# Kernel tuning notes

Measured on AMD Instinct MI355X. Metric: run time of the kernel, lower is better.

The kernel has to match this reference:

```python
import jax, jax.numpy as jnp
import numpy as np

B, S, C = 8, 4096, 256
K = 8192  # num_embeddings


def setup_inputs() -> dict:
    key = jax.random.key(0)
    k1, k2 = jax.random.split(key)
    inputs = jax.random.normal(k1, (B, S, C), dtype=jnp.float32)
    # torch init: uniform_(-1/K, 1/K)
    weight = jax.random.uniform(k2, (K, C), dtype=jnp.float32, minval=-1.0 / K, maxval=1.0 / K)
    return {"inputs": inputs, "weight": weight}


def reference(inputs, weight):
    b, s, c = inputs.shape
    flat = inputs.reshape(b * s, c)                       # (N, C)
    distances = (
        jnp.sum(flat * flat, axis=1, keepdims=True)
        + jnp.sum(weight * weight, axis=1)
        - 2.0 * jnp.matmul(flat, weight.T)
    )
    encoding_indices = jnp.argmin(distances, axis=1)      # (N,)
    quantized = weight[encoding_indices].reshape(b, s, c)  # gather == one-hot matmul
    encoding_indices = encoding_indices.reshape(b, s)
    # straight-through estimator
    quantized = inputs + jax.lax.stop_gradient(quantized - inputs)
    return quantized, encoding_indices
```

## Files before the change

kernel.cpp:

```cpp
#include <hip/hip_runtime.h>
#include <hip/hip_fp16.h>

#define N_ROWS 32768
#define KCODES 8192
#define CDIM   256
#define NSUB   (KCODES / 16)
#define MARGIN_DOT 2.2e-4f
#define CAP_ROW 15
#define CAP_BIN 1024

typedef __attribute__((ext_vector_type(8))) short bf16x8;
typedef __attribute__((ext_vector_type(4))) float f32x4;

#define GLOAD_LDS16(g, l)                                                              \
    __builtin_amdgcn_global_load_lds((const __attribute__((address_space(1))) void*)(g), \
                                     (__attribute__((address_space(3))) void*)(l), 16, 0, 0)

__device__ __forceinline__ ushort f2bf_rne(float f) {
    unsigned u = __float_as_uint(f);
    u += 0x7fffu + ((u >> 16) & 1u);
    return (ushort)(u >> 16);
}

__global__ void prep_kernel(const float* __restrict__ x, const float* __restrict__ wgt,
                            ushort* __restrict__ xb, ushort* __restrict__ wb,
                            float* __restrict__ t1, float* __restrict__ e2,
                            unsigned long long* __restrict__ bestG) {
    const int gtid = blockIdx.x * blockDim.x + threadIdx.x;
    if (gtid < N_ROWS) bestG[gtid] = ~0ull;

    int wave = gtid >> 6;
    int lane = threadIdx.x & 63;
    const float* src; ushort* bdst; float* sqdst; int row;
    if (wave < N_ROWS) { src = x; bdst = xb; sqdst = t1; row = wave; }
    else               { src = wgt; bdst = wb; sqdst = e2; row = wave - N_ROWS; }
    float4 v = *((const float4*)src + (size_t)row * (CDIM / 4) + lane);
    ushort4 o;
    o.x = f2bf_rne(v.x); o.y = f2bf_rne(v.y); o.z = f2bf_rne(v.z); o.w = f2bf_rne(v.w);
    *((ushort4*)bdst + (size_t)row * (CDIM / 4) + lane) = o;
    float s = v.x * v.x + v.y * v.y + v.z * v.z + v.w * v.w;
    for (int off = 32; off; off >>= 1) s += __shfl_down(s, off, 64);
    if (lane == 0) sqdst[row] = s;
}

__launch_bounds__(512, 3)
__global__ void vq_mfma_kernel(const ushort* __restrict__ xb, const ushort* __restrict__ wb,
                               __half* __restrict__ minT) {
    __shared__ ushort xs[2][256 * 32];
    __shared__ ushort ws_l[2][128 * 32];
    ushort (*mbT)[264] = (ushort (*)[264])&xs[0][0];

    const int t = threadIdx.x;
    const int w = t >> 6, lane = t & 63;
    const int ln15 = lane & 15, quad = lane >> 4;
    const int rt = blockIdx.x >> 6;
    const int ct = blockIdx.x & 63;
    const int rbase = (w >> 1) * 64;
    const int cbase = (w & 1) * 64;

    const int srow16 = lane >> 2;
    const int schunk = (lane & 3) ^ ((lane >> 3) & 3);
    const ushort* xsrc = xb + (size_t)(rt * 256 + w * 32 + srow16) * CDIM + schunk * 8;
    const ushort* wsrc = wb + (size_t)(ct * 128 + w * 16 + srow16) * CDIM + schunk * 8;

    f32x4 acc[4][4];
#pragma unroll
    for (int ni = 0; ni < 4; ++ni)
#pragma unroll
        for (int mi = 0; mi < 4; ++mi)
#pragma unroll
            for (int r = 0; r < 4; ++r) acc[ni][mi][r] = 0.f;

#pragma unroll
    for (int j = 0; j < 2; ++j)
        GLOAD_LDS16(xsrc + (size_t)j * 16 * CDIM, &xs[0][(w * 32 + j * 16) * 32]);
    GLOAD_LDS16(wsrc, &ws_l[0][(w * 16) * 32]);
    __syncthreads();

#pragma unroll
    for (int cc = 0; cc < 8; ++cc) {
        const int cur = cc & 1;
        if (cc < 7) {
#pragma unroll
            for (int j = 0; j < 2; ++j)
                GLOAD_LDS16(xsrc + (size_t)j * 16 * CDIM + (cc + 1) * 32,
                            &xs[cur ^ 1][(w * 32 + j * 16) * 32]);
            GLOAD_LDS16(wsrc + (cc + 1) * 32, &ws_l[cur ^ 1][(w * 16) * 32]);
        }
        const int swz = (quad ^ ((ln15 >> 1) & 3)) * 8;
        bf16x8 a[4], b[4];
#pragma unroll
        for (int ni = 0; ni < 4; ++ni)
            a[ni] = *(const bf16x8*)&ws_l[cur][(cbase + ni * 16 + ln15) * 32 + swz];
#pragma unroll
        for (int mi = 0; mi < 4; ++mi)
            b[mi] = *(const bf16x8*)&xs[cur][(rbase + mi * 16 + ln15) * 32 + swz];
#pragma unroll
        for (int ni = 0; ni < 4; ++ni)
#pragma unroll
            for (int mi = 0; mi < 4; ++mi)
                acc[ni][mi] = __builtin_amdgcn_mfma_f32_16x16x32_bf16(a[ni], b[mi], acc[ni][mi], 0, 0, 0);
        __syncthreads();
    }

#pragma unroll
    for (int mi = 0; mi < 4; ++mi) {
        float mxn[4];
#pragma unroll
        for (int ni = 0; ni < 4; ++ni) {
            f32x4 v = acc[ni][mi];
            float mx = fmaxf(fmaxf(v[0], v[1]), fmaxf(v[2], v[3]));
            mx = fmaxf(mx, __shfl_xor(mx, 16, 64));
            mx = fmaxf(mx, __shfl_xor(mx, 32, 64));
            mxn[ni] = mx;
        }
        float sel = quad == 0 ? mxn[0] : quad == 1 ? mxn[1] : quad == 2 ? mxn[2] : mxn[3];
        uint pk = __builtin_bit_cast(uint, __builtin_amdgcn_cvt_pkrtz(sel, sel));
        mbT[(cbase >> 4) + quad][rbase + mi * 16 + ln15] = (ushort)(pk & 0xffffu);
    }
    __syncthreads();
    if (t < 256) {
        union { ushort s[8]; uint4 u; } r;
#pragma unroll
        for (int s = 0; s < 8; ++s) r.s[s] = mbT[s][t];
        *(uint4*)(minT + ((size_t)(rt * 64 + ct) * 256 + t) * 8) = r.u;
    }
}

__launch_bounds__(256, 8)
__global__ void vq_scan_kernel(const __half* __restrict__ minT, uint* __restrict__ rowcand) {
    __shared__ ushort sm[64][136];
    __shared__ ushort cand[16][16];
    const int t = threadIdx.x, w = t >> 6, lane = t & 63;
    const int row0 = blockIdx.x * 16;

    {
        const int ct = t >> 2, c4 = t & 3;
        const uint4* src = (const uint4*)(minT +
            ((((size_t)(row0 >> 8) * 64 + ct) * 256 + (row0 & 255) + c4 * 4) * 8));
#pragma unroll
        for (int i = 0; i < 4; ++i)
            *(uint4*)&sm[ct][(c4 * 4 + i) * 8] = src[i];
    }
    __syncthreads();

    for (int i = 0; i < 4; ++i) {
        const int rr = w * 4 + i;
        union { uint4 u; __half2 h2[4]; } raw;
        raw.u = *(const uint4*)&sm[lane][rr * 8];
        float m[8];
#pragma unroll
        for (int q = 0; q < 4; ++q) {
            float2 f = __half22float2(raw.h2[q]);
            m[2 * q] = f.x;
            m[2 * q + 1] = f.y;
        }
        float lmax = m[0];
#pragma unroll
        for (int q = 1; q < 8; ++q) lmax = fmaxf(lmax, m[q]);
#pragma unroll
        for (int off = 1; off < 64; off <<= 1) lmax = fmaxf(lmax, __shfl_xor(lmax, off, 64));
        const float thresh = lmax - MARGIN_DOT;

        int base = 0;
#pragma unroll
        for (int s = 0; s < 8; ++s) {
            bool c = (m[s] >= thresh);
            unsigned long long mask = __ballot(c);
            if (c) {
                int pos = base + (int)__popcll(mask & ((1ull << lane) - 1ull));
                if (pos < CAP_ROW) cand[rr][1 + pos] = (ushort)(lane * 8 + s);
            }
            base += (int)__popcll(mask);
        }
        if (lane == 0) cand[rr][0] = (base <= CAP_ROW) ? (ushort)base : (ushort)0xffff;
    }
    __syncthreads();
    if (t < 128)
        rowcand[(size_t)(row0 + (t >> 3)) * 8 + (t & 7)] = ((const uint*)cand)[t];
}

__launch_bounds__(512, 4)
__global__ void vq_subproc_kernel(const float* __restrict__ x, const float* __restrict__ wgt,
                                  const float* __restrict__ t1, const float* __restrict__ e2,
                                  const uint* __restrict__ rowcand,
                                  unsigned long long* __restrict__ bestG) {
    __shared__ float wsub[16][260];
    __shared__ float xbuf[32][264];
    __shared__ int list[CAP_BIN];
    __shared__ int nlist;

    const int t = threadIdx.x;
    const int g = t >> 4, gl = t & 15;
    const int st = blockIdx.x;

    if (t == 0) nlist = 0;
#pragma unroll
    for (int j = 0; j < 2; ++j) {
        const int idx = t + 512 * j;
        *(float4*)&wsub[idx >> 6][(idx & 63) * 4] =
            ((const float4*)(wgt + (size_t)(st * 16 + (idx >> 6)) * CDIM))[idx & 63];
    }
    const float e2v = e2[st * 16 + gl];
    __syncthreads();

    for (int it = 0; it < 64; ++it) {
        const int r = t + 512 * it;
        union { struct { uint4 a, b; } qq; ushort h[16]; } rc;
        rc.qq.a = ((const uint4*)rowcand)[(size_t)r * 2];
        rc.qq.b = ((const uint4*)rowcand)[(size_t)r * 2 + 1];
        const uint cnt = rc.h[0];
        bool match = (cnt == 0xffffu);
        const int n = cnt < (uint)CAP_ROW ? (int)cnt : CAP_ROW;
#pragma unroll
        for (int j = 0; j < CAP_ROW; ++j)
            match |= (j < n) && (rc.h[1 + j] == (ushort)st);
        if (match) {
            const int pos = atomicAdd(&nlist, 1);
            if (pos < CAP_BIN) {
                list[pos] = r;
            } else {
                const float* xp = x + (size_t)r * CDIM;
                const float t1r = t1[r];
                unsigned long long bk = ~0ull;
                for (int kk = 0; kk < 16; ++kk) {
                    float acc = 0.f;
                    for (int c = 0; c < CDIM; ++c) acc = fmaf(xp[c], wsub[kk][c], acc);
                    float d = (t1r + e2[st * 16 + kk]) - 2.0f * acc;
                    unsigned long long key =
                        ((unsigned long long)__float_as_uint(d) << 32) | (uint)(st * 16 + kk);
                    bk = key < bk ? key : bk;
                }
                atomicMin(&bestG[r], bk);
            }
        }
    }
    __syncthreads();

    const int cnt = nlist < CAP_BIN ? nlist : CAP_BIN;
    for (int base = 0; base < cnt; base += 32) {
        const int e = base + g;
        const bool valid = e < cnt;
        int row = 0;
        if (valid) {
            row = list[e];
            const float4* xs = (const float4*)(x + (size_t)row * CDIM);
#pragma unroll
            for (int j = 0; j < 4; ++j)
                *(float4*)&xbuf[g][(gl + 16 * j) * 4] = xs[gl + 16 * j];
        }
        unsigned long long key = ~0ull;
        if (valid) {
            float acc = 0.f;
#pragma unroll
            for (int c4 = 0; c4 < 64; ++c4) {
                const float4 wv = *(const float4*)&wsub[gl][c4 * 4];
                const float4 xv = *(const float4*)&xbuf[g][c4 * 4];
                acc = fmaf(xv.x, wv.x, acc);
                acc = fmaf(xv.y, wv.y, acc);
                acc = fmaf(xv.z, wv.z, acc);
                acc = fmaf(xv.w, wv.w, acc);
            }
            const int k = st * 16 + gl;
            float d = (t1[row] + e2v) - 2.0f * acc;
            key = ((unsigned long long)__float_as_uint(d) << 32) | (uint)k;
        }
#pragma unroll
        for (int off = 1; off < 16; off <<= 1) {
            unsigned long long ok = __shfl_xor(key, off, 64);
            key = ok < key ? ok : key;
        }
        if (gl == 0 && valid) atomicMin(&bestG[row], key);
    }
}

__launch_bounds__(256, 8)
__global__ void vq_gather_kernel(const float* __restrict__ wgt,
                                 const unsigned long long* __restrict__ bestG,
                                 float* __restrict__ out_q, float* __restrict__ out_i) {
    const int t = threadIdx.x;
    const int g = t >> 4, gl = t & 15;
    const int row = blockIdx.x * 16 + g;
    const int bk = (int)(uint)(bestG[row] & 0xffffffffu);
    if (gl == 0) out_i[row] = (float)bk;
    const float4* src = (const float4*)(wgt + (size_t)bk * CDIM);
    float4* dst = (float4*)(out_q + (size_t)row * CDIM);
#pragma unroll
    for (int j = 0; j < 4; ++j) dst[gl + 16 * j] = src[gl + 16 * j];
}

extern "C" void kernel_launch(void* const* d_in, const int* in_sizes, int n_in,
                              void* d_out, int out_size, void* d_ws, size_t ws_size,
                              hipStream_t stream) {
    const float* x = (const float*)d_in[0];
    const float* wgt = (const float*)d_in[1];

    float* out_q = (float*)d_out;
    float* out_i = out_q + (size_t)N_ROWS * CDIM;

    char* p = (char*)d_ws;
    float* e2 = (float*)p;                     p += (size_t)KCODES * 4;
    float* t1 = (float*)p;                     p += (size_t)N_ROWS * 4;
    __half* minT = (__half*)p;                 p += (size_t)N_ROWS * NSUB * 2;
    ushort* xb = (ushort*)p;                   p += (size_t)N_ROWS * CDIM * 2;
    ushort* wb = (ushort*)p;                   p += (size_t)KCODES * CDIM * 2;
    unsigned long long* bestG = (unsigned long long*)p; p += (size_t)N_ROWS * 8;
    uint* rowcand = (uint*)p;                  p += (size_t)N_ROWS * 32;

    prep_kernel<<<(N_ROWS + KCODES) / 4, 256, 0, stream>>>(x, wgt, xb, wb, t1, e2, bestG);
    vq_mfma_kernel<<<(N_ROWS / 256) * (KCODES / 128), 512, 0, stream>>>(xb, wb, minT);
    vq_scan_kernel<<<N_ROWS / 16, 256, 0, stream>>>(minT, rowcand);
    vq_subproc_kernel<<<NSUB, 512, 0, stream>>>(x, wgt, t1, e2, rowcand, bestG);
    vq_gather_kernel<<<N_ROWS / 16, 256, 0, stream>>>(wgt, bestG, out_q, out_i);
}
```

Measured before the change: 347.1 us.

## Replace per-row candidate lists with row thresholds and split subproc over rows

The scan kernel now only computes a per-row threshold (row max minus margin) instead of building capped candidate lists. The subproc kernel reads the minT sub-block maxima and the threshold directly to decide whether a row belongs to its 16-code subtile. Its grid is split four ways over rows to raise parallelism. This removes the candidate-list writes and the 15-way compare loop per row, and removes the per-row cap that forced overflow rows into every subtile. In exchange, each subproc block does strided 16-byte reads from minT and an extra threshold load per row.

```diff
diff --git a/kernel.cpp b/kernel.cpp
--- a/kernel.cpp
+++ b/kernel.cpp
@@ -6,8 +6,8 @@
 #define CDIM   256
 #define NSUB   (KCODES / 16)
 #define MARGIN_DOT 2.2e-4f
-#define CAP_ROW 15
 #define CAP_BIN 1024
+#define SPLIT  4
 
 typedef __attribute__((ext_vector_type(8))) short bf16x8;
 typedef __attribute__((ext_vector_type(4))) float f32x4;
@@ -128,9 +128,8 @@
 }
 
 __launch_bounds__(256, 8)
-__global__ void vq_scan_kernel(const __half* __restrict__ minT, uint* __restrict__ rowcand) {
+__global__ void vq_rowmax_kernel(const __half* __restrict__ minT, float* __restrict__ thresh) {
     __shared__ ushort sm[64][136];
-    __shared__ ushort cand[16][16];
     const int t = threadIdx.x, w = t >> 6, lane = t & 63;
     const int row0 = blockIdx.x * 16;
 
@@ -160,30 +159,15 @@
         for (int q = 1; q < 8; ++q) lmax = fmaxf(lmax, m[q]);
 #pragma unroll
         for (int off = 1; off < 64; off <<= 1) lmax = fmaxf(lmax, __shfl_xor(lmax, off, 64));
-        const float thresh = lmax - MARGIN_DOT;
-
-        int base = 0;
-#pragma unroll
-        for (int s = 0; s < 8; ++s) {
-            bool c = (m[s] >= thresh);
-            unsigned long long mask = __ballot(c);
-            if (c) {
-                int pos = base + (int)__popcll(mask & ((1ull << lane) - 1ull));
-                if (pos < CAP_ROW) cand[rr][1 + pos] = (ushort)(lane * 8 + s);
-            }
-            base += (int)__popcll(mask);
-        }
-        if (lane == 0) cand[rr][0] = (base <= CAP_ROW) ? (ushort)base : (ushort)0xffff;
-    }
-    __syncthreads();
-    if (t < 128)
-        rowcand[(size_t)(row0 + (t >> 3)) * 8 + (t & 7)] = ((const uint*)cand)[t];
+        if (lane == 0) thresh[row0 + rr] = lmax - MARGIN_DOT;
+    }
 }
 
 __launch_bounds__(512, 4)
 __global__ void vq_subproc_kernel(const float* __restrict__ x, const float* __restrict__ wgt,
                                   const float* __restrict__ t1, const float* __restrict__ e2,
-                                  const uint* __restrict__ rowcand,
+                                  const __half* __restrict__ minT,
+                                  const float* __restrict__ thresh,
                                   unsigned long long* __restrict__ bestG) {
     __shared__ float wsub[16][260];
     __shared__ float xbuf[32][264];
@@ -192,7 +176,9 @@
 
     const int t = threadIdx.x;
     const int g = t >> 4, gl = t & 15;
-    const int st = blockIdx.x;
+    const int st = blockIdx.x >> 2;
+    const int sp = blockIdx.x & (SPLIT - 1);
+    const int ct = st >> 3, sub = st & 7;
 
     if (t == 0) nlist = 0;
 #pragma unroll
@@ -204,18 +190,15 @@
     const float e2v = e2[st * 16 + gl];
     __syncthreads();
 
-    for (int it = 0; it < 64; ++it) {
-        const int r = t + 512 * it;
-        union { struct { uint4 a, b; } qq; ushort h[16]; } rc;
-        rc.qq.a = ((const uint4*)rowcand)[(size_t)r * 2];
-        rc.qq.b = ((const uint4*)rowcand)[(size_t)r * 2 + 1];
-        const uint cnt = rc.h[0];
-        bool match = (cnt == 0xffffu);
-        const int n = cnt < (uint)CAP_ROW ? (int)cnt : CAP_ROW;
-#pragma unroll
-        for (int j = 0; j < CAP_ROW; ++j)
-            match |= (j < n) && (rc.h[1 + j] == (ushort)st);
-        if (match) {
+    for (int it = 0; it < 16; ++it) {
+        const int r = sp * (N_ROWS / SPLIT) + t + 512 * it;
+        const uint4 mg = *(const uint4*)(minT +
+            ((((size_t)(r >> 8) * 64 + ct) * 256 + (r & 255)) * 8));
+        const uint word = (sub >> 1) == 0 ? mg.x : (sub >> 1) == 1 ? mg.y
+                        : (sub >> 1) == 2 ? mg.z : mg.w;
+        const ushort hbits = (sub & 1) ? (ushort)(word >> 16) : (ushort)(word & 0xffffu);
+        const float ms = __half2float(__builtin_bit_cast(__half, hbits));
+        if (ms >= thresh[r]) {
             const int pos = atomicAdd(&nlist, 1);
             if (pos < CAP_BIN) {
                 list[pos] = r;
@@ -305,11 +288,11 @@
     ushort* xb = (ushort*)p;                   p += (size_t)N_ROWS * CDIM * 2;
     ushort* wb = (ushort*)p;                   p += (size_t)KCODES * CDIM * 2;
     unsigned long long* bestG = (unsigned long long*)p; p += (size_t)N_ROWS * 8;
-    uint* rowcand = (uint*)p;                  p += (size_t)N_ROWS * 32;
+    float* thresh = (float*)p;                 p += (size_t)N_ROWS * 4;
 
     prep_kernel<<<(N_ROWS + KCODES) / 4, 256, 0, stream>>>(x, wgt, xb, wb, t1, e2, bestG);
     vq_mfma_kernel<<<(N_ROWS / 256) * (KCODES / 128), 512, 0, stream>>>(xb, wb, minT);
-    vq_scan_kernel<<<N_ROWS / 16, 256, 0, stream>>>(minT, rowcand);
-    vq_subproc_kernel<<<NSUB, 512, 0, stream>>>(x, wgt, t1, e2, rowcand, bestG);
+    vq_rowmax_kernel<<<N_ROWS / 16, 256, 0, stream>>>(minT, thresh);
+    vq_subproc_kernel<<<NSUB * SPLIT, 512, 0, stream>>>(x, wgt, t1, e2, minT, thresh, bestG);
     vq_gather_kernel<<<N_ROWS / 16, 256, 0, stream>>>(wgt, bestG, out_q, out_i);
 }
```

Result: faster. 304.0 us (-12.4%).
